# Kernel tuning notes

Hardware: AMD Instinct MI355X
Metric: run time of the kernel (lower is better)

Reference implementation:

```python
import jax, jax.numpy as jnp
import numpy as np
import math

D, H, B, T = 1024, 16, 2, 2048
DH = D // H


def setup_inputs() -> dict:
    key = jax.random.key(0)
    ks = jax.random.split(key, 9)
    s = 1.0 / math.sqrt(D)
    x = jax.random.normal(ks[0], (B, T, D), dtype=jnp.float32)
    # True = masked position (masked_fill semantics); causal mask broadcast over b, h
    mask = jnp.triu(jnp.ones((T, T), dtype=bool), k=1)[None, None, :, :]
    wq = jax.random.normal(ks[1], (D, D), dtype=jnp.float32) * s
    bq = jnp.zeros((D,), dtype=jnp.float32)
    wk = jax.random.normal(ks[2], (D, D), dtype=jnp.float32) * s
    bk = jnp.zeros((D,), dtype=jnp.float32)
    wv = jax.random.normal(ks[3], (D, D), dtype=jnp.float32) * s
    bv = jnp.zeros((D,), dtype=jnp.float32)
    wo = jax.random.normal(ks[4], (D, D), dtype=jnp.float32) * s
    bo = jnp.zeros((D,), dtype=jnp.float32)
    return {"x": x, "mask": mask, "wq": wq, "bq": bq, "wk": wk, "bk": bk,
            "wv": wv, "bv": bv, "wo": wo, "bo": bo}


def _rotate_half(u):
    h = u.shape[-1] // 2
    return jnp.concatenate([-u[..., h:], u[..., :h]], axis=-1)


def _sincos(t, dh, dtype):
    pos = jnp.arange(t, dtype=dtype)[:, None]                    # [t, 1]
    inv = 1.0 / (10000.0 ** (jnp.arange(0, dh, 2, dtype=dtype) / dh))  # [dh/2]
    ang = pos * inv                                              # [t, dh/2]
    sin = jnp.repeat(jnp.sin(ang), 2, axis=-1)                   # [t, dh]
    cos = jnp.repeat(jnp.cos(ang), 2, axis=-1)
    return sin, cos


def reference(x, mask, wq, bq, wk, bk, wv, bv, wo, bo):
    b, t, d = x.shape
    h, dh = H, DH
    def heads(u):  # [b,t,d] -> [b,h,t,dh]
        return u.reshape(b, t, h, dh).transpose(0, 2, 1, 3)
    q = heads(x @ wq + bq)
    k = heads(x @ wk + bk)
    v = heads(x @ wv + bv)
    sin, cos = _sincos(t, dh, x.dtype)                           # [t, dh]
    q = q * cos + _rotate_half(q) * sin
    k = k * cos + _rotate_half(k) * sin
    a = jnp.einsum('bhqd,bhkd->bhqk', q, k) / jnp.sqrt(jnp.asarray(dh, x.dtype))
    a = jnp.where(mask, jnp.asarray(-10000.0, x.dtype), a)
    a = jax.nn.softmax(a, axis=-1)                               # dropout p=0.0 -> identity
    out = jnp.einsum('bhqk,bhkd->bhqd', a, v)
    out = out.transpose(0, 2, 1, 3).reshape(b, t, d)
    return out @ wo + bo
```

## Files before the change

kernel.cpp:

```cpp
#include <hip/hip_runtime.h>
#include <hip/hip_bf16.h>

#define DD 1024
#define HH 16
#define BB 2
#define TT 2048
#define DHH 64
#define MM (BB * TT)
#define NQT (TT / 64)
#define BKG 32

typedef __attribute__((ext_vector_type(8))) short bfrag;
typedef __attribute__((ext_vector_type(4))) float ffrag;

__device__ __forceinline__ unsigned short f2bf(float f) {
    __hip_bfloat16 h = __float2bfloat16(f);
    return *reinterpret_cast<unsigned short*>(&h);
}

__device__ __forceinline__ void gl_lds16(const unsigned short* g, unsigned short* l) {
    __builtin_amdgcn_global_load_lds(
        (const __attribute__((address_space(1))) unsigned int*)g,
        (__attribute__((address_space(3))) unsigned int*)l, 16, 0, 0);
}

__global__ __launch_bounds__(256) void prepass_kernel(
    const float* __restrict__ x, unsigned short* __restrict__ xb,
    const float* __restrict__ wq, const float* __restrict__ wk,
    const float* __restrict__ wv, const float* __restrict__ wo,
    unsigned short* __restrict__ oq, unsigned short* __restrict__ ok,
    unsigned short* __restrict__ ov, unsigned short* __restrict__ oo,
    float4* __restrict__ rope_tab)
{
    __shared__ float T[64][65];
    const int z = blockIdx.z;
    const int t = threadIdx.x;
    if (z == 4) {
        const int bid = blockIdx.y * 16 + blockIdx.x;
#pragma unroll
        for (int g = 0; g < 16; ++g) {
            int i = bid * 4096 + g * 256 + t;
            float4 v = ((const float4*)x)[i];
            ushort4 o;
            o.x = f2bf(v.x); o.y = f2bf(v.y); o.z = f2bf(v.z); o.w = f2bf(v.w);
            ((ushort4*)xb)[i] = o;
        }
        int idx = bid * 256 + t;
        int tpos = idx >> 5, i = idx & 31;
        float inv = __expf(-(float)i * (9.210340371976184f / 32.0f));
        float ang = (float)tpos * inv;
        float sv, cv;
        sincosf(ang, &sv, &cv);
        const float S = 0.125f * 1.4426950408889634f;
        rope_tab[idx] = make_float4(cv, sv, S * cv, S * sv);
        return;
    }
    const float* W    = (z == 0) ? wq : (z == 1) ? wk : (z == 2) ? wv : wo;
    unsigned short* O = (z == 0) ? oq : (z == 1) ? ok : (z == 2) ? ov : oo;
    const int n0 = blockIdx.x * 64, k0 = blockIdx.y * 64;
#pragma unroll
    for (int g = 0; g < 16; ++g) {
        int idx = g * 256 + t;
        int r = idx >> 6, c = idx & 63;
        T[c][r] = W[(size_t)(k0 + r) * DD + n0 + c];
    }
    __syncthreads();
#pragma unroll
    for (int g = 0; g < 16; ++g) {
        int idx = g * 256 + t;
        int r = idx >> 6, c = idx & 63;
        O[(size_t)(n0 + r) * DD + k0 + c] = f2bf(T[r][c]);
    }
}

__device__ __forceinline__ void gemm128(
    const unsigned short* __restrict__ X, const unsigned short* __restrict__ Wt,
    int m0, int n0, unsigned short* As, unsigned short* Bs, ffrag acc[4][4])
{
    const int t  = threadIdx.x;
    const int l  = t & 63, w = t >> 6;
    const int lm = l & 15, lq = l >> 4;
    const int wr = w >> 1, wc = w & 1;
    const int srow = l >> 2;
    const int scol = (l & 3) * 8;
#pragma unroll
    for (int m = 0; m < 4; ++m)
#pragma unroll
        for (int n = 0; n < 4; ++n) acc[m][n] = (ffrag){0.f, 0.f, 0.f, 0.f};

    for (int k0 = 0; k0 < DD; k0 += BKG) {
#pragma unroll
        for (int it = 0; it < 2; ++it) {
            const int row = (w * 2 + it) * 16 + srow;
            gl_lds16(&X [(size_t)(m0 + row) * DD + k0 + scol], &As[(w * 2 + it) * 512]);
            gl_lds16(&Wt[(size_t)(n0 + row) * DD + k0 + scol], &Bs[(w * 2 + it) * 512]);
        }
        __syncthreads();
        bfrag a[4], b[4];
#pragma unroll
        for (int m = 0; m < 4; ++m)
            a[m] = *(const bfrag*)&As[(wr * 64 + m * 16 + lm) * BKG + lq * 8];
#pragma unroll
        for (int n = 0; n < 4; ++n)
            b[n] = *(const bfrag*)&Bs[(wc * 64 + n * 16 + lm) * BKG + lq * 8];
#pragma unroll
        for (int m = 0; m < 4; ++m)
#pragma unroll
            for (int n = 0; n < 4; ++n)
                acc[m][n] = __builtin_amdgcn_mfma_f32_16x16x32_bf16(a[m], b[n], acc[m][n], 0, 0, 0);
        __syncthreads();
    }
}

__global__ __launch_bounds__(256) void qkv_rope_kernel(
    const unsigned short* __restrict__ xb,
    const unsigned short* __restrict__ wt_qkv,
    const float* __restrict__ bq, const float* __restrict__ bk,
    const float* __restrict__ bv, const float4* __restrict__ rope_tab,
    unsigned short* __restrict__ Qh, unsigned short* __restrict__ Kh,
    unsigned short* __restrict__ Vh)
{
    __shared__ __align__(16) unsigned short As[128 * BKG];
    __shared__ __align__(16) unsigned short Bs[128 * BKG];
    const int n0 = blockIdx.x * 128, m0 = blockIdx.y * 128;
    ffrag acc[4][4];
    gemm128(xb, wt_qkv, m0, n0, As, Bs, acc);

    const int t  = threadIdx.x;
    const int l  = t & 63, w = t >> 6;
    const int lm = l & 15, lq = l >> 4;
    const int wr = w >> 1, wc = w & 1;
    const int ncol0 = n0 + wc * 64;
    const int which = ncol0 >> 10;
    const float* bias   = (which == 0) ? bq : (which == 1) ? bk : bv;
    unsigned short* Out = (which == 0) ? Qh : (which == 1) ? Kh : Vh;
    const int h = (ncol0 & 1023) >> 6;

    float bv4[4];
#pragma unroll
    for (int n = 0; n < 4; ++n) bv4[n] = bias[(ncol0 & 1023) + n * 16 + lm];

#pragma unroll
    for (int m = 0; m < 4; ++m) {
#pragma unroll
        for (int r = 0; r < 4; ++r) {
            const int row  = m0 + wr * 64 + m * 16 + lq * 4 + r;
            const int b    = row >> 11;
            const int tpos = row & 2047;
            const int bh   = b * HH + h;
#pragma unroll
            for (int n = 0; n < 4; ++n) {
                const int j = n * 16 + lm;
                float val = acc[m][n][r] + bv4[n];
                float outv;
                if (which < 2) {
                    float pair = acc[m][n ^ 2][r] + bv4[n ^ 2];
                    float rh   = (j < 32) ? -pair : pair;
                    float4 cs  = rope_tab[tpos * 32 + (j >> 1)];
                    outv = (which == 0) ? (val * cs.z + rh * cs.w)
                                        : (val * cs.x + rh * cs.y);
                } else {
                    outv = val;
                }
                Out[((size_t)bh * TT + tpos) * DHH + j] = f2bf(outv);
            }
        }
    }
}

__global__ __launch_bounds__(256) void attn_kernel(
    const unsigned short* __restrict__ Qh, const unsigned short* __restrict__ Kh,
    const unsigned short* __restrict__ Vh, unsigned short* __restrict__ attn_out)
{
    __shared__ __align__(16) unsigned short Ks[2][64][72];
    __shared__ __align__(16) unsigned short Vt[2][64][72];

    const int fid = (int)blockIdx.y * 16 + (int)blockIdx.x;
    const int xcd = fid & 7, j = fid >> 3;
    const int bh  = ((j >> 4) << 3) + xcd;
    const int bx  = j & 15;

    const int t  = threadIdx.x;
    const int l  = t & 63, w = t >> 6;
    const int lm = l & 15, lq = l >> 4;
    const int g  = t >> 3;
    const int c0 = (t & 7) * 8;

    const unsigned short* Qb = Qh + (size_t)bh * TT * DHH;
    const unsigned short* Kb = Kh + (size_t)bh * TT * DHH;
    const unsigned short* Vb = Vh + (size_t)bh * TT * DHH;

    const bfrag onesf = (bfrag){0x3F80, 0x3F80, 0x3F80, 0x3F80,
                                0x3F80, 0x3F80, 0x3F80, 0x3F80};
    const int b = bh >> 4, h = bh & 15;
    const int srcA = (2 * (lq & 1)) * 16 + lm;
    const int srcB = srcA + 16;
    const bool sig = (lq >> 1) != 0;

#pragma unroll 1
    for (int pi = 0; pi < 2; ++pi) {
        const int qt  = (pi == 0) ? (NQT - 1 - bx) : bx;
        const int q0  = qt * 64, wm0 = q0 + w * 16;
        const int rowg = wm0 + lm;

        bfrag qf[2];
#pragma unroll
        for (int kc = 0; kc < 2; ++kc)
            qf[kc] = *(const bfrag*)&Qb[(size_t)(wm0 + lm) * DHH + kc * 32 + lq * 8];

        ffrag o[4];
#pragma unroll
        for (int s = 0; s < 4; ++s) o[s] = (ffrag){0.f, 0.f, 0.f, 0.f};
        ffrag lacc = (ffrag){0.f, 0.f, 0.f, 0.f};

        {
            uint4 ka  = *(const uint4*)&Kb[(size_t)(g) * DHH + c0];
            uint4 kb2 = *(const uint4*)&Kb[(size_t)(g + 32) * DHH + c0];
            uint4 va  = *(const uint4*)&Vb[(size_t)(2 * g) * DHH + c0];
            uint4 vb2 = *(const uint4*)&Vb[(size_t)(2 * g + 1) * DHH + c0];
            *(uint4*)&Ks[0][g][c0]      = ka;
            *(uint4*)&Ks[0][g + 32][c0] = kb2;
            const unsigned short* as = (const unsigned short*)&va;
            const unsigned short* bs = (const unsigned short*)&vb2;
#pragma unroll
            for (int jj = 0; jj < 8; ++jj) {
                unsigned int wp = (unsigned int)as[jj] | ((unsigned int)bs[jj] << 16);
                const int dh = c0 + jj;
                const int ch = (g >> 2) ^ ((dh >> 3) & 7);
                *(unsigned int*)&Vt[0][dh][ch * 8 + (g & 3) * 2] = wp;
            }
        }
        __syncthreads();

        const int nkt = qt + 1;
#pragma unroll 1
        for (int kt = 0; kt < nkt; ++kt) {
            const int cur = kt & 1;
            const bool pf = (kt < qt);
            uint4 ka, kb2, va, vb2;
            if (pf) {
                const int k1 = (kt + 1) * 64;
                ka  = *(const uint4*)&Kb[(size_t)(k1 + g) * DHH + c0];
                kb2 = *(const uint4*)&Kb[(size_t)(k1 + g + 32) * DHH + c0];
                va  = *(const uint4*)&Vb[(size_t)(k1 + 2 * g) * DHH + c0];
                vb2 = *(const uint4*)&Vb[(size_t)(k1 + 2 * g + 1) * DHH + c0];
            }
            const int k0 = kt * 64;

            float sv[4][4];
            __builtin_amdgcn_s_setprio(1);
#pragma unroll
            for (int s = 0; s < 4; ++s) {
                ffrag sa = (ffrag){0.f, 0.f, 0.f, 0.f};
#pragma unroll
                for (int kc = 0; kc < 2; ++kc) {
                    bfrag kf = *(const bfrag*)&Ks[cur][s * 16 + lm][kc * 32 + lq * 8];
                    sa = __builtin_amdgcn_mfma_f32_16x16x32_bf16(kf, qf[kc], sa, 0, 0, 0);
                }
#pragma unroll
                for (int r = 0; r < 4; ++r) sv[s][r] = sa[r];
            }
            __builtin_amdgcn_s_setprio(0);
            if (kt == qt) {
#pragma unroll
                for (int s = 0; s < 4; ++s)
#pragma unroll
                    for (int r = 0; r < 4; ++r) {
                        const int col = k0 + s * 16 + lq * 4 + r;
                        if (col > rowg) sv[s][r] = -1e30f;
                    }
            }
#pragma unroll
            for (int s = 0; s < 4; ++s)
#pragma unroll
                for (int r = 0; r < 4; ++r)
                    sv[s][r] = __builtin_amdgcn_exp2f(sv[s][r]);

            unsigned int pk[8];
#pragma unroll
            for (int s = 0; s < 4; ++s)
#pragma unroll
                for (int p = 0; p < 2; ++p)
                    asm("v_cvt_pk_bf16_f32 %0, %1, %2"
                        : "=v"(pk[s * 2 + p])
                        : "v"(sv[s][2 * p]), "v"(sv[s][2 * p + 1]));

            uint4 paw[2];
#pragma unroll
            for (int kc = 0; kc < 2; ++kc)
#pragma unroll
                for (int m = 0; m < 4; ++m) {
                    const int src = (m & 2) ? srcB : srcA;
                    unsigned int w0 = (unsigned int)__shfl((int)pk[kc * 4 + (m & 1)], src, 64);
                    unsigned int w1 = (unsigned int)__shfl((int)pk[kc * 4 + 2 + (m & 1)], src, 64);
                    ((unsigned int*)&paw[kc])[m] = sig ? w1 : w0;
                }

            __builtin_amdgcn_s_setprio(1);
#pragma unroll
            for (int kc = 0; kc < 2; ++kc) {
                bfrag pa = *(const bfrag*)&paw[kc];
#pragma unroll
                for (int s = 0; s < 4; ++s) {
                    const int ch = (kc * 4 + lq) ^ ((s * 2 + (lm >> 3)) & 7);
                    bfrag vf = *(const bfrag*)&Vt[cur][s * 16 + lm][ch * 8];
                    o[s] = __builtin_amdgcn_mfma_f32_16x16x32_bf16(pa, vf, o[s], 0, 0, 0);
                }
                lacc = __builtin_amdgcn_mfma_f32_16x16x32_bf16(pa, onesf, lacc, 0, 0, 0);
            }
            __builtin_amdgcn_s_setprio(0);

            if (pf) {
                const int nxt = cur ^ 1;
                *(uint4*)&Ks[nxt][g][c0]      = ka;
                *(uint4*)&Ks[nxt][g + 32][c0] = kb2;
                const unsigned short* as = (const unsigned short*)&va;
                const unsigned short* bs = (const unsigned short*)&vb2;
#pragma unroll
                for (int jj = 0; jj < 8; ++jj) {
                    unsigned int wp = (unsigned int)as[jj] | ((unsigned int)bs[jj] << 16);
                    const int dh = c0 + jj;
                    const int ch = (g >> 2) ^ ((dh >> 3) & 7);
                    *(unsigned int*)&Vt[nxt][dh][ch * 8 + (g & 3) * 2] = wp;
                }
            }
            __syncthreads();
        }

#pragma unroll
        for (int r = 0; r < 4; ++r) {
            const int trow = wm0 + lq * 4 + r;
            const float linv = 1.0f / lacc[r];
#pragma unroll
            for (int s = 0; s < 4; ++s) {
                float ov = o[s][r] * linv;
                attn_out[(((size_t)b * TT + trow) * HH + h) * DHH + s * 16 + lm] = f2bf(ov);
            }
        }
        __syncthreads();
    }
}

__global__ __launch_bounds__(256) void oproj_kernel(
    const unsigned short* __restrict__ attn, const unsigned short* __restrict__ wto,
    const float* __restrict__ bo, float* __restrict__ out)
{
    __shared__ __align__(16) unsigned short As[128 * BKG];
    __shared__ __align__(16) unsigned short Bs[64 * BKG];
    const int n0 = blockIdx.x * 64, m0 = blockIdx.y * 128;
    const int t  = threadIdx.x;
    const int l  = t & 63, w = t >> 6;
    const int lm = l & 15, lq = l >> 4;

    ffrag acc[2][4];
#pragma unroll
    for (int m = 0; m < 2; ++m)
#pragma unroll
        for (int n = 0; n < 4; ++n) acc[m][n] = (ffrag){0.f, 0.f, 0.f, 0.f};

    for (int k0 = 0; k0 < DD; k0 += BKG) {
        {
            int c = t;
            gl_lds16(&attn[(size_t)(m0 + (c >> 2)) * DD + k0 + (c & 3) * 8], &As[c * 8]);
            c = t + 256;
            gl_lds16(&attn[(size_t)(m0 + (c >> 2)) * DD + k0 + (c & 3) * 8], &As[c * 8]);
            gl_lds16(&wto [(size_t)(n0 + (t >> 2)) * DD + k0 + (t & 3) * 8], &Bs[t * 8]);
        }
        __syncthreads();
        bfrag a[2], b[4];
#pragma unroll
        for (int m = 0; m < 2; ++m)
            a[m] = *(const bfrag*)&As[(w * 32 + m * 16 + lm) * BKG + lq * 8];
#pragma unroll
        for (int n = 0; n < 4; ++n)
            b[n] = *(const bfrag*)&Bs[(n * 16 + lm) * BKG + lq * 8];
#pragma unroll
        for (int m = 0; m < 2; ++m)
#pragma unroll
            for (int n = 0; n < 4; ++n)
                acc[m][n] = __builtin_amdgcn_mfma_f32_16x16x32_bf16(a[m], b[n], acc[m][n], 0, 0, 0);
        __syncthreads();
    }

#pragma unroll
    for (int n = 0; n < 4; ++n) {
        const int col = n0 + n * 16 + lm;
        const float bb = bo[col];
#pragma unroll
        for (int m = 0; m < 2; ++m)
#pragma unroll
            for (int r = 0; r < 4; ++r) {
                const int row = m0 + w * 32 + m * 16 + lq * 4 + r;
                out[(size_t)row * DD + col] = acc[m][n][r] + bb;
            }
    }
}

extern "C" void kernel_launch(void* const* d_in, const int* in_sizes, int n_in,
                              void* d_out, int out_size, void* d_ws, size_t ws_size,
                              hipStream_t stream) {
    const float* x  = (const float*)d_in[0];
    const float* wq = (const float*)d_in[2];
    const float* bq = (const float*)d_in[3];
    const float* wk = (const float*)d_in[4];
    const float* bk = (const float*)d_in[5];
    const float* wv = (const float*)d_in[6];
    const float* bv = (const float*)d_in[7];
    const float* wo = (const float*)d_in[8];
    const float* bo = (const float*)d_in[9];

    const size_t perT = (size_t)BB * HH * TT * DHH;
    const size_t perW = (size_t)DD * DD;
    unsigned short* xb   = (unsigned short*)d_ws;
    unsigned short* wtq  = xb  + perT;
    unsigned short* wtk  = wtq + perW;
    unsigned short* wtv  = wtk + perW;
    unsigned short* wto  = wtv + perW;
    unsigned short* Qh   = wto + perW;
    unsigned short* Kh   = Qh + perT;
    unsigned short* Vh   = Kh + perT;
    unsigned short* attn = Vh + perT;
    float4* rope_tab     = (float4*)(attn + perT);

    prepass_kernel<<<dim3(16, 16, 5), 256, 0, stream>>>(
        x, xb, wq, wk, wv, wo, wtq, wtk, wtv, wto, rope_tab);
    qkv_rope_kernel<<<dim3(24, 32), 256, 0, stream>>>(
        xb, wtq, bq, bk, bv, rope_tab, Qh, Kh, Vh);
    attn_kernel<<<dim3(NQT / 2, 32), 256, 0, stream>>>(Qh, Kh, Vh, attn);
    oproj_kernel<<<dim3(16, 32), 256, 0, stream>>>(attn, wto, bo, (float*)d_out);
}
```

Baseline: 214.4 us.

## Shrink attention blocks to 32 query rows with 128 threads, doubling grid

```diff
diff --git a/kernel.cpp b/kernel.cpp
--- a/kernel.cpp
+++ b/kernel.cpp
@@ -168,17 +168,17 @@
     }
 }
 
-__global__ __launch_bounds__(256) void attn_kernel(
+__global__ __launch_bounds__(128) void attn_kernel(
     const unsigned short* __restrict__ Qh, const unsigned short* __restrict__ Kh,
     const unsigned short* __restrict__ Vh, unsigned short* __restrict__ attn_out)
 {
     __shared__ __align__(16) unsigned short Ks[2][64][72];
     __shared__ __align__(16) unsigned short Vt[2][64][72];
 
-    const int fid = (int)blockIdx.y * 16 + (int)blockIdx.x;
+    const int fid = (int)blockIdx.y * 32 + (int)blockIdx.x;
     const int xcd = fid & 7, j = fid >> 3;
-    const int bh  = ((j >> 4) << 3) + xcd;
-    const int bx  = j & 15;
+    const int bh  = ((j >> 5) << 3) + xcd;
+    const int bx  = j & 31;
 
     const int t  = threadIdx.x;
     const int l  = t & 63, w = t >> 6;
@@ -199,8 +199,8 @@
 
 #pragma unroll 1
     for (int pi = 0; pi < 2; ++pi) {
-        const int qt  = (pi == 0) ? (NQT - 1 - bx) : bx;
-        const int q0  = qt * 64, wm0 = q0 + w * 16;
+        const int qt  = (pi == 0) ? (63 - bx) : bx;
+        const int q0  = qt * 32, wm0 = q0 + w * 16;
         const int rowg = wm0 + lm;
 
         bfrag qf[2];
@@ -213,37 +213,53 @@
         for (int s = 0; s < 4; ++s) o[s] = (ffrag){0.f, 0.f, 0.f, 0.f};
         ffrag lacc = (ffrag){0.f, 0.f, 0.f, 0.f};
 
+        const int nkt = (qt >> 1) + 1;
+
         {
-            uint4 ka  = *(const uint4*)&Kb[(size_t)(g) * DHH + c0];
-            uint4 kb2 = *(const uint4*)&Kb[(size_t)(g + 32) * DHH + c0];
-            uint4 va  = *(const uint4*)&Vb[(size_t)(2 * g) * DHH + c0];
-            uint4 vb2 = *(const uint4*)&Vb[(size_t)(2 * g + 1) * DHH + c0];
-            *(uint4*)&Ks[0][g][c0]      = ka;
-            *(uint4*)&Ks[0][g + 32][c0] = kb2;
-            const unsigned short* as = (const unsigned short*)&va;
-            const unsigned short* bs = (const unsigned short*)&vb2;
+            uint4 ka0 = *(const uint4*)&Kb[(size_t)(g) * DHH + c0];
+            uint4 ka1 = *(const uint4*)&Kb[(size_t)(g + 16) * DHH + c0];
+            uint4 ka2 = *(const uint4*)&Kb[(size_t)(g + 32) * DHH + c0];
+            uint4 ka3 = *(const uint4*)&Kb[(size_t)(g + 48) * DHH + c0];
+            uint4 va0 = *(const uint4*)&Vb[(size_t)(4 * g) * DHH + c0];
+            uint4 va1 = *(const uint4*)&Vb[(size_t)(4 * g + 1) * DHH + c0];
+            uint4 va2 = *(const uint4*)&Vb[(size_t)(4 * g + 2) * DHH + c0];
+            uint4 va3 = *(const uint4*)&Vb[(size_t)(4 * g + 3) * DHH + c0];
+            *(uint4*)&Ks[0][g][c0]      = ka0;
+            *(uint4*)&Ks[0][g + 16][c0] = ka1;
+            *(uint4*)&Ks[0][g + 32][c0] = ka2;
+            *(uint4*)&Ks[0][g + 48][c0] = ka3;
+            const unsigned short* a0 = (const unsigned short*)&va0;
+            const unsigned short* a1 = (const unsigned short*)&va1;
+            const unsigned short* a2 = (const unsigned short*)&va2;
+            const unsigned short* a3 = (const unsigned short*)&va3;
+            const int j1 = 2 * g, j2 = 2 * g + 1;
 #pragma unroll
             for (int jj = 0; jj < 8; ++jj) {
-                unsigned int wp = (unsigned int)as[jj] | ((unsigned int)bs[jj] << 16);
                 const int dh = c0 + jj;
-                const int ch = (g >> 2) ^ ((dh >> 3) & 7);
-                *(unsigned int*)&Vt[0][dh][ch * 8 + (g & 3) * 2] = wp;
-            }
-        }
-        __syncthreads();
-
-        const int nkt = qt + 1;
+                const int cb = (dh >> 3) & 7;
+                unsigned int wp1 = (unsigned int)a0[jj] | ((unsigned int)a1[jj] << 16);
+                *(unsigned int*)&Vt[0][dh][((j1 >> 2) ^ cb) * 8 + (j1 & 3) * 2] = wp1;
+                unsigned int wp2 = (unsigned int)a2[jj] | ((unsigned int)a3[jj] << 16);
+                *(unsigned int*)&Vt[0][dh][((j2 >> 2) ^ cb) * 8 + (j2 & 3) * 2] = wp2;
+            }
+        }
+        __syncthreads();
+
 #pragma unroll 1
         for (int kt = 0; kt < nkt; ++kt) {
             const int cur = kt & 1;
-            const bool pf = (kt < qt);
-            uint4 ka, kb2, va, vb2;
+            const bool pf = (kt + 1 < nkt);
+            uint4 ka0, ka1, ka2, ka3, va0, va1, va2, va3;
             if (pf) {
                 const int k1 = (kt + 1) * 64;
-                ka  = *(const uint4*)&Kb[(size_t)(k1 + g) * DHH + c0];
-                kb2 = *(const uint4*)&Kb[(size_t)(k1 + g + 32) * DHH + c0];
-                va  = *(const uint4*)&Vb[(size_t)(k1 + 2 * g) * DHH + c0];
-                vb2 = *(const uint4*)&Vb[(size_t)(k1 + 2 * g + 1) * DHH + c0];
+                ka0 = *(const uint4*)&Kb[(size_t)(k1 + g) * DHH + c0];
+                ka1 = *(const uint4*)&Kb[(size_t)(k1 + g + 16) * DHH + c0];
+                ka2 = *(const uint4*)&Kb[(size_t)(k1 + g + 32) * DHH + c0];
+                ka3 = *(const uint4*)&Kb[(size_t)(k1 + g + 48) * DHH + c0];
+                va0 = *(const uint4*)&Vb[(size_t)(k1 + 4 * g) * DHH + c0];
+                va1 = *(const uint4*)&Vb[(size_t)(k1 + 4 * g + 1) * DHH + c0];
+                va2 = *(const uint4*)&Vb[(size_t)(k1 + 4 * g + 2) * DHH + c0];
+                va3 = *(const uint4*)&Vb[(size_t)(k1 + 4 * g + 3) * DHH + c0];
             }
             const int k0 = kt * 64;
 
@@ -261,7 +277,7 @@
                 for (int r = 0; r < 4; ++r) sv[s][r] = sa[r];
             }
             __builtin_amdgcn_s_setprio(0);
-            if (kt == qt) {
+            if (kt == nkt - 1) {
 #pragma unroll
                 for (int s = 0; s < 4; ++s)
 #pragma unroll
@@ -312,16 +328,23 @@
 
             if (pf) {
                 const int nxt = cur ^ 1;
-                *(uint4*)&Ks[nxt][g][c0]      = ka;
-                *(uint4*)&Ks[nxt][g + 32][c0] = kb2;
-                const unsigned short* as = (const unsigned short*)&va;
-                const unsigned short* bs = (const unsigned short*)&vb2;
+                *(uint4*)&Ks[nxt][g][c0]      = ka0;
+                *(uint4*)&Ks[nxt][g + 16][c0] = ka1;
+                *(uint4*)&Ks[nxt][g + 32][c0] = ka2;
+                *(uint4*)&Ks[nxt][g + 48][c0] = ka3;
+                const unsigned short* a0 = (const unsigned short*)&va0;
+                const unsigned short* a1 = (const unsigned short*)&va1;
+                const unsigned short* a2 = (const unsigned short*)&va2;
+                const unsigned short* a3 = (const unsigned short*)&va3;
+                const int j1 = 2 * g, j2 = 2 * g + 1;
 #pragma unroll
                 for (int jj = 0; jj < 8; ++jj) {
-                    unsigned int wp = (unsigned int)as[jj] | ((unsigned int)bs[jj] << 16);
                     const int dh = c0 + jj;
-                    const int ch = (g >> 2) ^ ((dh >> 3) & 7);
-                    *(unsigned int*)&Vt[nxt][dh][ch * 8 + (g & 3) * 2] = wp;
+                    const int cb = (dh >> 3) & 7;
+                    unsigned int wp1 = (unsigned int)a0[jj] | ((unsigned int)a1[jj] << 16);
+                    *(unsigned int*)&Vt[nxt][dh][((j1 >> 2) ^ cb) * 8 + (j1 & 3) * 2] = wp1;
+                    unsigned int wp2 = (unsigned int)a2[jj] | ((unsigned int)a3[jj] << 16);
+                    *(unsigned int*)&Vt[nxt][dh][((j2 >> 2) ^ cb) * 8 + (j2 & 3) * 2] = wp2;
                 }
             }
             __syncthreads();
@@ -426,6 +449,6 @@
         x, xb, wq, wk, wv, wo, wtq, wtk, wtv, wto, rope_tab);
     qkv_rope_kernel<<<dim3(24, 32), 256, 0, stream>>>(
         xb, wtq, bq, bk, bv, rope_tab, Qh, Kh, Vh);
-    attn_kernel<<<dim3(NQT / 2, 32), 256, 0, stream>>>(Qh, Kh, Vh, attn);
+    attn_kernel<<<dim3(32, 32), 128, 0, stream>>>(Qh, Kh, Vh, attn);
     oproj_kernel<<<dim3(16, 32), 256, 0, stream>>>(attn, wto, bo, (float*)d_out);
 }
```

New measurement: 223.3 us. +4.2%, slower.
